# Performance work log

Measured on AMD Instinct MI355X. Metric: run time of the kernel, lower is better.

## Reference

```python
import jax, jax.numpy as jnp
from jax import lax
import numpy as np

_BN_SCALE = 1.0 / float(np.sqrt(1.0 + 1e-5))  # eval BN: running_mean=0, running_var=1
SEMANTIC_GROUPS = [
    ("head_spine", [0, 1, 2, 3, 20]),
    ("left_arm", [4, 5, 6, 7, 21, 22]),
    ("right_arm", [8, 9, 10, 11, 23, 24]),
    ("left_leg", [12, 13, 14, 15]),
    ("right_leg", [16, 17, 18, 19]),
]
_SKELETON_EDGES = [(3, 2), (2, 20), (20, 1), (1, 0), (20, 4), (4, 5), (5, 6), (6, 22), (6, 7), (7, 21),
                   (20, 8), (8, 9), (9, 10), (10, 24), (10, 11), (11, 23), (0, 12), (12, 13), (13, 14),
                   (14, 15), (0, 16), (16, 17), (17, 18), (18, 19)]


def _full_adj():
    adj = np.zeros((25, 25))
    for i, j in [(a - 1, b - 1) for a, b in _SKELETON_EDGES]:
        if 0 <= i < 25 and 0 <= j < 25:
            adj[i, j] = 1.0
            adj[j, i] = 1.0
    adj += np.eye(25)
    deg = adj.sum(1, keepdims=True)
    deg[deg == 0] = 1.0
    return adj / deg


def _sub_adj(joints):
    fa = _full_adj()
    sa = fa[np.ix_(joints, joints)].copy()
    n = len(joints)
    if n > 1:
        sa += np.eye(n)
        deg = sa.sum(1)
        for node in np.nonzero(deg == 1.0)[0]:
            if node != 0:
                sa[0, node] = 1.0
                sa[node, 0] = 1.0
    deg = sa.sum(1, keepdims=True)
    deg[deg == 0] = 1.0
    return jnp.asarray((sa / deg).astype(np.float32))


def _bn(y, g, b):
    # eval-mode BatchNorm2d with running stats (0, 1)
    return y * (g * _BN_SCALE)[None, :, None, None] + b[None, :, None, None]


def _st_layer(x, adj, sw, sb, tw, tb, g, b, res):
    # x: (B, Cin, T, V); sw: (3*Cout, Cin); tw: (Cout, Cout, 3, 1)
    if res is None:
        r = x
    else:
        rw, rb, rg, rbb = res
        r = _bn(jnp.einsum('oc,bctv->botv', rw, x) + rb[None, :, None, None], rg, rbb)
    xg = jnp.einsum('uv,bctv->bctu', adj, x)  # adjacency message passing
    y = jnp.einsum('oc,bctv->botv', sw, xg) + sb[None, :, None, None]
    B, oc3, T, V = y.shape
    y = y.reshape(B, 3, oc3 // 3, T, V).sum(axis=1)  # sum spatial kernel partitions
    y = lax.conv_general_dilated(y, tw, (1, 1), ((1, 1), (0, 0))) + tb[None, :, None, None]
    return jax.nn.relu(_bn(y + r, g, b))


def _vq(inp, cb):
    # inp: (B, D), cb: (K, D); straight-through VQ with commitment_cost=0.25
    d = jnp.sum(inp * inp, 1, keepdims=True) + jnp.sum(cb * cb, 1) - 2.0 * (inp @ cb.T)
    idx = jnp.argmin(d, axis=1)
    q = cb[idx]
    sg = lax.stop_gradient
    loss = jnp.mean((q - sg(inp)) ** 2) + 0.25 * jnp.mean((sg(q) - inp) ** 2)
    return inp + sg(q - inp), loss, idx


def _forward(x, embed_w, embed_b, p1, p2, p3, codebooks):
    h = jnp.einsum('btvc,oc->btvo', x, embed_w) + embed_b  # (B,T,25,64)
    h = h.transpose(0, 3, 1, 2)  # (B,64,T,25)
    quants, losses, idxs = [], [], []
    for gi, (_, joints) in enumerate(SEMANTIC_GROUPS):
        adj = _sub_adj(joints)
        y = h[:, :, :, np.asarray(joints)]
        sw1, sb1, tw1, tb1, g1, b1 = [p[gi] for p in p1]
        y = _st_layer(y, adj, sw1, sb1, tw1, tb1, g1, b1, None)
        rw2, rb2, rg2, rbb2, sw2, sb2, tw2, tb2, g2, b2 = [p[gi] for p in p2]
        y = _st_layer(y, adj, sw2, sb2, tw2, tb2, g2, b2, (rw2, rb2, rg2, rbb2))
        rw3, rb3, rg3, rbb3, sw3, sb3, tw3, tb3, g3, b3 = [p[gi] for p in p3]
        y = _st_layer(y, adj, sw3, sb3, tw3, tb3, g3, b3, (rw3, rb3, rg3, rbb3))
        feat = y.mean(axis=(2, 3))  # AdaptiveAvgPool2d((1,1))
        q, l, i = _vq(feat, codebooks[gi])
        quants.append(q)
        losses.append(l)
        idxs.append(i)
    return jnp.stack(quants), jnp.sum(jnp.stack(losses)), jnp.stack(idxs)


def setup_inputs() -> dict:
    ks = iter(jax.random.split(jax.random.key(0), 48))

    def rn(shape, scale=0.05):
        return jax.random.normal(next(ks), shape, jnp.float32) * scale

    return {
        "x": jax.random.normal(next(ks), (64, 256, 25, 3), jnp.float32),
        "embed_w": rn((64, 3), 0.3),
        "embed_b": rn((64,), 0.01),
        "sgcn_w1": rn((5, 192, 64)),
        "sgcn_b1": rn((5, 192), 0.01),
        "tconv_w1": rn((5, 64, 64, 3, 1)),
        "tconv_b1": rn((5, 64), 0.01),
        "bn_g1": jnp.ones((5, 64), jnp.float32),
        "bn_b1": jnp.zeros((5, 64), jnp.float32),
        "res_w2": rn((5, 128, 64)),
        "res_b2": rn((5, 128), 0.01),
        "resbn_g2": jnp.ones((5, 128), jnp.float32),
        "resbn_b2": jnp.zeros((5, 128), jnp.float32),
        "sgcn_w2": rn((5, 384, 64)),
        "sgcn_b2": rn((5, 384), 0.01),
        "tconv_w2": rn((5, 128, 128, 3, 1)),
        "tconv_b2": rn((5, 128), 0.01),
        "bn_g2": jnp.ones((5, 128), jnp.float32),
        "bn_b2": jnp.zeros((5, 128), jnp.float32),
        "res_w3": rn((5, 64, 128)),
        "res_b3": rn((5, 64), 0.01),
        "resbn_g3": jnp.ones((5, 64), jnp.float32),
        "resbn_b3": jnp.zeros((5, 64), jnp.float32),
        "sgcn_w3": rn((5, 192, 128)),
        "sgcn_b3": rn((5, 192), 0.01),
        "tconv_w3": rn((5, 64, 64, 3, 1)),
        "tconv_b3": rn((5, 64), 0.01),
        "bn_g3": jnp.ones((5, 64), jnp.float32),
        "bn_b3": jnp.zeros((5, 64), jnp.float32),
        "codebooks": jax.random.uniform(next(ks), (5, 128, 64), jnp.float32, -1.0 / 128, 1.0 / 128),
    }


def reference(x, embed_w, embed_b, sgcn_w1, sgcn_b1, tconv_w1, tconv_b1, bn_g1, bn_b1,
              res_w2, res_b2, resbn_g2, resbn_b2, sgcn_w2, sgcn_b2, tconv_w2, tconv_b2, bn_g2, bn_b2,
              res_w3, res_b3, resbn_g3, resbn_b3, sgcn_w3, sgcn_b3, tconv_w3, tconv_b3, bn_g3, bn_b3,
              codebooks):
    p1 = (sgcn_w1, sgcn_b1, tconv_w1, tconv_b1, bn_g1, bn_b1)
    p2 = (res_w2, res_b2, resbn_g2, resbn_b2, sgcn_w2, sgcn_b2, tconv_w2, tconv_b2, bn_g2, bn_b2)
    p3 = (res_w3, res_b3, resbn_g3, resbn_b3, sgcn_w3, sgcn_b3, tconv_w3, tconv_b3, bn_g3, bn_b3)
    return _forward(x, embed_w, embed_b, p1, p2, p3, codebooks)
```

## Files before the change

kernel.cpp:

```cpp
#include <hip/hip_runtime.h>

#define T_ 256
#define B_ 64
static constexpr float BNS = 0.9999950000374997f;

__device__ __constant__ int d_perm[25] = {0,1,2,3,20, 4,5,6,7,21,22, 8,9,10,11,23,24, 12,13,14,15, 16,17,18,19};
__device__ __constant__ int d_gstart[5] = {0,5,11,17,21};
__device__ __constant__ int d_gn[5] = {5,6,6,4,4};
__device__ __constant__ int d_edges[21][2] = {
  {2,1},{1,19},{19,0},{19,3},{3,4},{4,5},{5,21},{5,6},{6,20},{19,7},
  {7,8},{8,9},{9,23},{9,10},{10,22},{11,12},{12,13},{13,14},{15,16},{16,17},{17,18}};

__global__ void adj_kernel(float* __restrict__ adjout){
  if (threadIdx.x != 0 || blockIdx.x != 0) return;
  double fa[25][25];
  for (int i=0;i<25;i++) for (int j=0;j<25;j++) fa[i][j]=0.0;
  for (int e=0;e<21;e++){ int i=d_edges[e][0], j=d_edges[e][1]; fa[i][j]=1.0; fa[j][i]=1.0; }
  for (int i=0;i<25;i++) fa[i][i] += 1.0;
  for (int i=0;i<25;i++){
    double dg=0; for (int j=0;j<25;j++) dg += fa[i][j];
    if (dg==0.0) dg=1.0;
    for (int j=0;j<25;j++) fa[i][j] /= dg;
  }
  for (int g=0; g<5; g++){
    int n = d_gn[g]; int gs = d_gstart[g];
    for (int q=0;q<36;q++) adjout[g*36+q] = 0.f;
    double sa[6][6];
    for (int a=0;a<n;a++) for (int b=0;b<n;b++) sa[a][b] = fa[d_perm[gs+a]][d_perm[gs+b]];
    for (int a=0;a<n;a++) sa[a][a] += 1.0;
    double deg[6];
    for (int a=0;a<n;a++){ double s=0; for (int b=0;b<n;b++) s += sa[a][b]; deg[a]=s; }
    for (int a=1;a<n;a++) if (deg[a]==1.0){ sa[0][a]=1.0; sa[a][0]=1.0; }
    for (int a=0;a<n;a++){
      double s=0; for (int b=0;b<n;b++) s += sa[a][b];
      if (s==0.0) s=1.0;
      for (int b=0;b<n;b++) adjout[g*36 + a*n + b] = (float)(sa[a][b]/s);
    }
  }
}

__global__ void zero_kernel(float* __restrict__ feat, float* __restrict__ loss){
  int i = blockIdx.x*256 + threadIdx.x;
  if (i < 5*64*64) feat[i] = 0.f;
  if (i == 0) loss[0] = 0.f;
}

__global__ __launch_bounds__(256) void fold_swe(
    const float* __restrict__ sw1, const float* __restrict__ sw2, const float* __restrict__ sw3,
    float* __restrict__ swe1, float* __restrict__ swe2, float* __restrict__ swe3){
  int i = blockIdx.x*256 + threadIdx.x;
  if (i < 20480){ int g=i/4096, r=i%4096;
    swe1[i] = sw1[g*12288 + r] + sw1[g*12288 + 4096 + r] + sw1[g*12288 + 8192 + r];
  } else if (i < 61440){ int j=i-20480; int g=j/8192, r=j%8192;
    swe2[j] = sw2[g*24576 + r] + sw2[g*24576 + 8192 + r] + sw2[g*24576 + 16384 + r];
  } else if (i < 102400){ int j=i-61440; int g=j/8192, r=j%8192;
    swe3[j] = sw3[g*24576 + r] + sw3[g*24576 + 8192 + r] + sw3[g*24576 + 16384 + r];
  }
}

template<int Cm, int Cout>
__global__ __launch_bounds__(256) void transpose_tw(const float* __restrict__ tw, float* __restrict__ twT){
  int e = blockIdx.x*256 + threadIdx.x;
  if (e >= 5*3*Cm*Cout) return;
  int o = e % Cout;
  int t = e / Cout;
  int m = t % Cm; t /= Cm;
  int k = t % 3; int g = t/3;
  twT[e] = tw[(size_t)g*Cout*Cm*3 + (o*Cm+m)*3 + k];
}

template<int Cm, int Cin, int Cout>
__global__ __launch_bounds__(256) void prep_gemm(
    const float* __restrict__ twT, const float* __restrict__ swe,
    const float* __restrict__ bg, float* __restrict__ WC){
  constexpr int CT = 256/Cout;
  __shared__ float sS[Cm*CT];
  int g = blockIdx.x, k = blockIdx.y, cz = blockIdx.z;
  int tid = threadIdx.x;
  for (int i=tid; i<Cm*CT; i+=256){
    int m = i/CT, cc = i%CT;
    sS[i] = swe[(size_t)g*Cm*Cin + m*Cin + cz*CT + cc];
  }
  __syncthreads();
  int o = tid % Cout, cc = tid / Cout;
  const float* tp = twT + ((size_t)(g*3+k)*Cm)*Cout + o;
  float acc = 0.f;
  #pragma unroll 4
  for (int m=0;m<Cm;m++) acc += tp[(size_t)m*Cout]*sS[m*CT+cc];
  int c = cz*CT + cc;
  WC[(size_t)g*3*Cin*Cout + ((size_t)k*Cin + c)*Cout + o] = bg[g*Cout+o]*BNS*acc;
}

__global__ __launch_bounds__(256) void prep_rw(
    const float* __restrict__ rw2, const float* __restrict__ rg2, const float* __restrict__ bg2,
    const float* __restrict__ rw3, const float* __restrict__ rg3, const float* __restrict__ bg3,
    float* __restrict__ RW2, float* __restrict__ RW3){
  int i = blockIdx.x*256 + threadIdx.x;
  if (i < 40960){ int g=i/8192, r=i%8192, c=r>>7, o=r&127;
    RW2[i] = bg2[g*128+o]*BNS*rg2[g*128+o]*BNS*rw2[(size_t)g*8192 + o*64 + c];
  } else if (i < 81920){ int j=i-40960; int g=j/8192, r=j%8192, c=r>>6, o=r&63;
    RW3[j] = bg3[g*64+o]*BNS*rg3[g*64+o]*BNS*rw3[(size_t)g*8192 + o*128 + c];
  }
}

__global__ __launch_bounds__(128) void prep_bias(
    const float* __restrict__ twT1, const float* __restrict__ twT2, const float* __restrict__ twT3,
    const float* __restrict__ sb1, const float* __restrict__ tb1, const float* __restrict__ bg1, const float* __restrict__ bb1,
    const float* __restrict__ sb2, const float* __restrict__ tb2, const float* __restrict__ bg2, const float* __restrict__ bb2,
    const float* __restrict__ rb2, const float* __restrict__ rg2, const float* __restrict__ rbb2,
    const float* __restrict__ sb3, const float* __restrict__ tb3, const float* __restrict__ bg3, const float* __restrict__ bb3,
    const float* __restrict__ rb3, const float* __restrict__ rg3, const float* __restrict__ rbb3,
    float* __restrict__ B1, float* __restrict__ RS1, float* __restrict__ B2, float* __restrict__ B3){
  __shared__ float sbe[128];
  int g = blockIdx.x, L = blockIdx.y, tid = threadIdx.x;
  if (L == 0){
    if (tid<64) sbe[tid] = sb1[g*192+tid] + sb1[g*192+64+tid] + sb1[g*192+128+tid];
    __syncthreads();
    if (tid<64){ int o=tid; float gsc = bg1[g*64+o]*BNS;
      for (int k=0;k<3;k++){ float s=0.f; const float* tp = twT1 + ((size_t)(g*3+k)*64)*64 + o;
        for (int m=0;m<64;m++) s += tp[m*64]*sbe[m];
        B1[g*256+(k+1)*64+o] = gsc*s; }
      B1[g*256+o] = gsc*tb1[g*64+o] + bb1[g*64+o];
      RS1[g*64+o] = gsc;
    }
  } else if (L == 1){
    sbe[tid] = sb2[g*384+tid] + sb2[g*384+128+tid] + sb2[g*384+256+tid];
    __syncthreads();
    { int o=tid; float gsc = bg2[g*128+o]*BNS; float rgs = rg2[g*128+o]*BNS;
      for (int k=0;k<3;k++){ float s=0.f; const float* tp = twT2 + ((size_t)(g*3+k)*128)*128 + o;
        for (int m=0;m<128;m++) s += tp[m*128]*sbe[m];
        B2[g*512+(k+1)*128+o] = gsc*s; }
      B2[g*512+o] = gsc*(tb2[g*128+o] + rgs*rb2[g*128+o] + rbb2[g*128+o]) + bb2[g*128+o];
    }
  } else {
    if (tid<64) sbe[tid] = sb3[g*192+tid] + sb3[g*192+64+tid] + sb3[g*192+128+tid];
    __syncthreads();
    if (tid<64){ int o=tid; float gsc = bg3[g*64+o]*BNS; float rgs = rg3[g*64+o]*BNS;
      for (int k=0;k<3;k++){ float s=0.f; const float* tp = twT3 + ((size_t)(g*3+k)*64)*64 + o;
        for (int m=0;m<64;m++) s += tp[m*64]*sbe[m];
        B3[g*256+(k+1)*64+o] = gsc*s; }
      B3[g*256+o] = gsc*(tb3[g*64+o] + rgs*rb3[g*64+o] + rbb3[g*64+o]) + bb3[g*64+o];
    }
  }
}

template<int Cin, int Cout, int NJ, int MODE>
__global__ __launch_bounds__(256) void st_layer(
    const float* __restrict__ in, float* __restrict__ out,
    const float* __restrict__ W, const float* __restrict__ RW,
    const float* __restrict__ BV, const float* __restrict__ RS,
    const float* __restrict__ adjg, const float* __restrict__ ew,
    const float* __restrict__ eb, int gstart)
{
  constexpr int TC = 16;
  constexpr int SE = (TC+2)*NJ;
  constexpr int SITES = TC*NJ;
  constexpr int SP = SITES/8;
  constexpr int OP = Cout/32;
  __shared__ float sIn[SE*Cin];
  __shared__ float sXg[SE*Cin];
  __shared__ float sAdj[NJ*NJ];
  const int tid = threadIdx.x;
  const int b = blockIdx.y;
  const int t0 = blockIdx.x*TC;
  if (tid < NJ*NJ) sAdj[tid] = adjg[tid];

  if (MODE == 1){
    for (int e=tid; e<SE*3; e+=256){
      int se = e/3, j = e - se*3;
      int tl = se/NJ; int u = se - tl*NJ; int t = t0 + tl - 1;
      float v = 0.f;
      if (t>=0 && t<T_){ int joint = d_perm[gstart+u]; v = in[(((size_t)b*T_ + t)*25 + joint)*3 + j]; }
      sXg[e] = v;
    }
    __syncthreads();
    { int c = tid & 63;
      float w0 = ew[c*3], w1 = ew[c*3+1], w2 = ew[c*3+2], b0 = eb[c];
      for (int e=tid; e<SE*64; e+=256){
        int se = e>>6; int t = t0 + se/NJ - 1;
        float v = 0.f;
        if (t>=0 && t<T_) v = b0 + sXg[se*3]*w0 + sXg[se*3+1]*w1 + sXg[se*3+2]*w2;
        sIn[e] = v;
      }
    }
    __syncthreads();
  } else {
    constexpr int NV = SE*Cin/4;
    for (int e4=tid; e4<NV; e4+=256){
      int idx = e4*4;
      int se = idx/Cin; int cc = idx - se*Cin;
      int tl = se/NJ; int u = se - tl*NJ; int t = t0 + tl - 1;
      float4 v = make_float4(0.f,0.f,0.f,0.f);
      if (t>=0 && t<T_) v = *(const float4*)&in[(((size_t)b*T_ + t)*NJ + u)*Cin + cc];
      *(float4*)&sIn[idx] = v;
    }
    __syncthreads();
  }
  for (int e=tid; e<SE*Cin; e+=256){
    int se = e/Cin; int c = e - se*Cin;
    int u = se % NJ; int base = (se-u)*Cin + c;
    float a = 0.f;
    #pragma unroll
    for (int v=0; v<NJ; v++) a += sAdj[u*NJ+v]*sIn[base + v*Cin];
    sXg[e] = a;
  }
  __syncthreads();

  const int lane = tid & 63;
  const int o = lane & 31;
  const int sg = (tid>>6)*2 + (lane>>5);
  const int s0 = sg*SP;

  float acc[SP][OP];
  {
    float bno[OP], bk0[OP], bk1[OP], bk2[OP];
    #pragma unroll
    for (int j=0;j<OP;j++){ int oj = o + j*32;
      bno[j]=BV[oj]; bk0[j]=BV[Cout+oj]; bk1[j]=BV[2*Cout+oj]; bk2[j]=BV[3*Cout+oj]; }
    #pragma unroll
    for (int i=0;i<SP;i++){
      int s = s0 + i; int tg = t0 + s/NJ;
      #pragma unroll
      for (int j=0;j<OP;j++)
        acc[i][j] = bno[j] + bk1[j] + (tg>0 ? bk0[j] : 0.f) + (tg<T_-1 ? bk2[j] : 0.f);
    }
  }
  #pragma unroll 1
  for (int k=0;k<3;k++){
    const float* Wk = W + k*Cin*Cout;
    #pragma unroll 2
    for (int c4=0;c4<Cin;c4+=4){
      float wv[4][OP];
      #pragma unroll
      for (int q=0;q<4;q++)
        #pragma unroll
        for (int j=0;j<OP;j++) wv[q][j] = Wk[(c4+q)*Cout + o + j*32];
      #pragma unroll
      for (int i=0;i<SP;i++){
        const float4 xv = *(const float4*)&sXg[(s0+i+k*NJ)*Cin + c4];
        #pragma unroll
        for (int j=0;j<OP;j++)
          acc[i][j] += xv.x*wv[0][j] + xv.y*wv[1][j] + xv.z*wv[2][j] + xv.w*wv[3][j];
      }
    }
  }
  if (MODE == 1){
    float rsv[OP];
    #pragma unroll
    for (int j=0;j<OP;j++) rsv[j] = RS[o + j*32];
    #pragma unroll
    for (int i=0;i<SP;i++)
      #pragma unroll
      for (int j=0;j<OP;j++)
        acc[i][j] += sIn[(s0+i+NJ)*Cin + o + j*32]*rsv[j];
  } else {
    #pragma unroll 2
    for (int c4=0;c4<Cin;c4+=4){
      float rv[4][OP];
      #pragma unroll
      for (int q=0;q<4;q++)
        #pragma unroll
        for (int j=0;j<OP;j++) rv[q][j] = RW[(c4+q)*Cout + o + j*32];
      #pragma unroll
      for (int i=0;i<SP;i++){
        const float4 xv = *(const float4*)&sIn[(s0+i+NJ)*Cin + c4];
        #pragma unroll
        for (int j=0;j<OP;j++)
          acc[i][j] += xv.x*rv[0][j] + xv.y*rv[1][j] + xv.z*rv[2][j] + xv.w*rv[3][j];
      }
    }
  }
  if (MODE == 3){
    #pragma unroll
    for (int j=0;j<OP;j++){
      float sum = 0.f;
      #pragma unroll
      for (int i=0;i<SP;i++) sum += fmaxf(acc[i][j], 0.f);
      atomicAdd(&out[(size_t)b*64 + o + j*32], sum);
    }
  } else {
    size_t obase = ((size_t)b*T_ + t0)*NJ*Cout;
    #pragma unroll
    for (int i=0;i<SP;i++)
      #pragma unroll
      for (int j=0;j<OP;j++)
        out[obase + (size_t)(s0+i)*Cout + o + j*32] = fmaxf(acc[i][j], 0.f);
  }
}

__global__ __launch_bounds__(128) void vq_kernel(const float* __restrict__ feat,
    const float* __restrict__ cb, float* __restrict__ dout){
  int b = blockIdx.x, g = blockIdx.y, tid = threadIdx.x;
  __shared__ float sF[64];
  __shared__ float sD[128]; __shared__ int sI[128];
  __shared__ float sL[64];
  float inv = 1.0f/(256.0f*(float)d_gn[g]);
  if (tid < 64) sF[tid] = feat[((size_t)g*64 + b)*64 + tid]*inv;
  __syncthreads();
  const float* cbg = cb + (size_t)g*128*64;
  {
    const float* c = cbg + (size_t)tid*64;
    float d = 0.f;
    for (int i=0;i<64;i++){ float df = c[i]-sF[i]; d += df*df; }
    sD[tid] = d; sI[tid] = tid;
  }
  __syncthreads();
  for (int s=64; s>0; s>>=1){
    if (tid < s){
      float d2 = sD[tid+s]; int i2 = sI[tid+s];
      if (d2 < sD[tid] || (d2 == sD[tid] && i2 < sI[tid])){ sD[tid]=d2; sI[tid]=i2; }
    }
    __syncthreads();
  }
  int idx = sI[0];
  if (tid < 64){
    float q = cbg[(size_t)idx*64 + tid];
    dout[((size_t)g*64 + b)*64 + tid] = q;
    float df = q - sF[tid];
    sL[tid] = df*df;
  }
  __syncthreads();
  if (tid == 0){
    float s = 0.f;
    for (int i=0;i<64;i++) s += sL[i];
    atomicAdd(dout + 20480, 1.25f*s/4096.0f);
    dout[20481 + g*64 + b] = (float)idx;
  }
}

static void launch_st1(int nj, dim3 grid, hipStream_t s, const float* x, float* A1,
    const float* WC, const float* BV, const float* RS, const float* adj,
    const float* ew, const float* eb, int gstart){
  switch(nj){
    case 4: st_layer<64,64,4,1><<<grid,256,0,s>>>(x,A1,WC,nullptr,BV,RS,adj,ew,eb,gstart); break;
    case 5: st_layer<64,64,5,1><<<grid,256,0,s>>>(x,A1,WC,nullptr,BV,RS,adj,ew,eb,gstart); break;
    case 6: st_layer<64,64,6,1><<<grid,256,0,s>>>(x,A1,WC,nullptr,BV,RS,adj,ew,eb,gstart); break;
  }
}
static void launch_st2(int nj, dim3 grid, hipStream_t s, const float* A1, float* A2,
    const float* WC, const float* RW, const float* BV, const float* adj){
  switch(nj){
    case 4: st_layer<64,128,4,2><<<grid,256,0,s>>>(A1,A2,WC,RW,BV,nullptr,adj,nullptr,nullptr,0); break;
    case 5: st_layer<64,128,5,2><<<grid,256,0,s>>>(A1,A2,WC,RW,BV,nullptr,adj,nullptr,nullptr,0); break;
    case 6: st_layer<64,128,6,2><<<grid,256,0,s>>>(A1,A2,WC,RW,BV,nullptr,adj,nullptr,nullptr,0); break;
  }
}
static void launch_st3(int nj, dim3 grid, hipStream_t s, const float* A2, float* featg,
    const float* WC, const float* RW, const float* BV, const float* adj){
  switch(nj){
    case 4: st_layer<128,64,4,3><<<grid,256,0,s>>>(A2,featg,WC,RW,BV,nullptr,adj,nullptr,nullptr,0); break;
    case 5: st_layer<128,64,5,3><<<grid,256,0,s>>>(A2,featg,WC,RW,BV,nullptr,adj,nullptr,nullptr,0); break;
    case 6: st_layer<128,64,6,3><<<grid,256,0,s>>>(A2,featg,WC,RW,BV,nullptr,adj,nullptr,nullptr,0); break;
  }
}

extern "C" void kernel_launch(void* const* d_in, const int* in_sizes, int n_in,
                              void* d_out, int out_size, void* d_ws, size_t ws_size,
                              hipStream_t stream) {
  const float* x    = (const float*)d_in[0];
  const float* ew   = (const float*)d_in[1];
  const float* eb   = (const float*)d_in[2];
  const float* sw1  = (const float*)d_in[3];
  const float* sb1  = (const float*)d_in[4];
  const float* tw1  = (const float*)d_in[5];
  const float* tb1  = (const float*)d_in[6];
  const float* bg1  = (const float*)d_in[7];
  const float* bb1  = (const float*)d_in[8];
  const float* rw2  = (const float*)d_in[9];
  const float* rb2  = (const float*)d_in[10];
  const float* rg2  = (const float*)d_in[11];
  const float* rbb2 = (const float*)d_in[12];
  const float* sw2  = (const float*)d_in[13];
  const float* sb2  = (const float*)d_in[14];
  const float* tw2  = (const float*)d_in[15];
  const float* tb2  = (const float*)d_in[16];
  const float* bg2  = (const float*)d_in[17];
  const float* bb2  = (const float*)d_in[18];
  const float* rw3  = (const float*)d_in[19];
  const float* rb3  = (const float*)d_in[20];
  const float* rg3  = (const float*)d_in[21];
  const float* rbb3 = (const float*)d_in[22];
  const float* sw3  = (const float*)d_in[23];
  const float* sb3  = (const float*)d_in[24];
  const float* tw3  = (const float*)d_in[25];
  const float* tb3  = (const float*)d_in[26];
  const float* bg3  = (const float*)d_in[27];
  const float* bb3  = (const float*)d_in[28];
  const float* cbs  = (const float*)d_in[29];
  float* dout = (float*)d_out;
  float* ws = (float*)d_ws;

  const size_t OFF_ADJ = 0;
  const size_t OFF_WC1 = 256;
  const size_t OFF_B1  = 61696;
  const size_t OFF_RS1 = 62976;
  const size_t OFF_WC2 = 63296;
  const size_t OFF_RW2 = 186176;
  const size_t OFF_B2  = 227136;
  const size_t OFF_WC3 = 229696;
  const size_t OFF_RW3 = 352576;
  const size_t OFF_B3  = 393536;
  const size_t OFF_FEAT= 394816;
  const size_t OFF_A1  = 415296;
  const size_t OFF_A2  = 6706752;
  const size_t WS_FLOATS = 19289664;
  if (ws_size < WS_FLOATS*sizeof(float)) return;

  float* adj5 = ws + OFF_ADJ;
  float* WC1  = ws + OFF_WC1;  float* B1 = ws + OFF_B1;  float* RS1 = ws + OFF_RS1;
  float* WC2  = ws + OFF_WC2;  float* RW2 = ws + OFF_RW2; float* B2 = ws + OFF_B2;
  float* WC3  = ws + OFF_WC3;  float* RW3 = ws + OFF_RW3; float* B3 = ws + OFF_B3;
  float* feat = ws + OFF_FEAT;
  float* A1   = ws + OFF_A1;
  float* A2   = ws + OFF_A2;

  float* twT1 = A2;
  float* twT2 = A2 + 61440;
  float* twT3 = A2 + 307200;
  float* swe1 = A2 + 368640;
  float* swe2 = A2 + 389120;
  float* swe3 = A2 + 430080;

  zero_kernel<<<80, 256, 0, stream>>>(feat, dout + 20480);
  adj_kernel<<<1, 64, 0, stream>>>(adj5);
  fold_swe<<<400, 256, 0, stream>>>(sw1, sw2, sw3, swe1, swe2, swe3);
  transpose_tw<64,64>  <<<240, 256, 0, stream>>>(tw1, twT1);
  transpose_tw<128,128><<<960, 256, 0, stream>>>(tw2, twT2);
  transpose_tw<64,64>  <<<240, 256, 0, stream>>>(tw3, twT3);
  prep_gemm<64,64,64>  <<<dim3(5,3,16), 256, 0, stream>>>(twT1, swe1, bg1, WC1);
  prep_gemm<128,64,128><<<dim3(5,3,32), 256, 0, stream>>>(twT2, swe2, bg2, WC2);
  prep_gemm<64,128,64> <<<dim3(5,3,32), 256, 0, stream>>>(twT3, swe3, bg3, WC3);
  prep_rw<<<320, 256, 0, stream>>>(rw2, rg2, bg2, rw3, rg3, bg3, RW2, RW3);
  prep_bias<<<dim3(5,3), 128, 0, stream>>>(twT1, twT2, twT3,
      sb1, tb1, bg1, bb1,
      sb2, tb2, bg2, bb2, rb2, rg2, rbb2,
      sb3, tb3, bg3, bb3, rb3, rg3, rbb3,
      B1, RS1, B2, B3);

  const int h_gn[5] = {5,6,6,4,4};
  const int h_gstart[5] = {0,5,11,17,21};
  dim3 grid(T_/16, B_);
  for (int g=0; g<5; g++){
    int nj = h_gn[g];
    launch_st1(nj, grid, stream, x, A1, WC1 + (size_t)g*12288, B1 + g*256, RS1 + g*64,
               adj5 + g*36, ew, eb, h_gstart[g]);
    launch_st2(nj, grid, stream, A1, A2, WC2 + (size_t)g*24576, RW2 + (size_t)g*8192,
               B2 + g*512, adj5 + g*36);
    launch_st3(nj, grid, stream, A2, feat + (size_t)g*4096, WC3 + (size_t)g*24576,
               RW3 + (size_t)g*8192, B3 + g*256, adj5 + g*36);
  }
  vq_kernel<<<dim3(B_,5), 128, 0, stream>>>(feat, cbs, dout);
}
```

Before: 1.699 ms.

## Chunk input channels by 32 and split layer-2 outputs across grid z

```diff
diff --git a/kernel.cpp b/kernel.cpp
--- a/kernel.cpp
+++ b/kernel.cpp
@@ -144,8 +144,8 @@
   }
 }
 
-template<int Cin, int Cout, int NJ, int MODE>
-__global__ __launch_bounds__(256) void st_layer(
+template<int Cin, int COS, int NJ, int MODE>
+__global__ __launch_bounds__(256, 4) void st_layer(
     const float* __restrict__ in, float* __restrict__ out,
     const float* __restrict__ W, const float* __restrict__ RW,
     const float* __restrict__ BV, const float* __restrict__ RS,
@@ -156,55 +156,30 @@
   constexpr int SE = (TC+2)*NJ;
   constexpr int SITES = TC*NJ;
   constexpr int SP = SITES/8;
-  constexpr int OP = Cout/32;
-  __shared__ float sIn[SE*Cin];
-  __shared__ float sXg[SE*Cin];
+  constexpr int OP = 2;
+  constexpr int NCH = Cin/32;
+  __shared__ float sIn[SE*32];
+  __shared__ float sXg[SE*32];
   __shared__ float sAdj[NJ*NJ];
+  __shared__ float sX3[MODE==1 ? SE*3 : 1];
   const int tid = threadIdx.x;
   const int b = blockIdx.y;
   const int t0 = blockIdx.x*TC;
+  const int ooff = blockIdx.z*64;
+  W += ooff; BV += ooff;
+  if (MODE != 1) RW += ooff;
+  if (MODE == 2) out += ooff;
+
   if (tid < NJ*NJ) sAdj[tid] = adjg[tid];
-
   if (MODE == 1){
     for (int e=tid; e<SE*3; e+=256){
       int se = e/3, j = e - se*3;
       int tl = se/NJ; int u = se - tl*NJ; int t = t0 + tl - 1;
       float v = 0.f;
       if (t>=0 && t<T_){ int joint = d_perm[gstart+u]; v = in[(((size_t)b*T_ + t)*25 + joint)*3 + j]; }
-      sXg[e] = v;
-    }
-    __syncthreads();
-    { int c = tid & 63;
-      float w0 = ew[c*3], w1 = ew[c*3+1], w2 = ew[c*3+2], b0 = eb[c];
-      for (int e=tid; e<SE*64; e+=256){
-        int se = e>>6; int t = t0 + se/NJ - 1;
-        float v = 0.f;
-        if (t>=0 && t<T_) v = b0 + sXg[se*3]*w0 + sXg[se*3+1]*w1 + sXg[se*3+2]*w2;
-        sIn[e] = v;
-      }
-    }
-    __syncthreads();
-  } else {
-    constexpr int NV = SE*Cin/4;
-    for (int e4=tid; e4<NV; e4+=256){
-      int idx = e4*4;
-      int se = idx/Cin; int cc = idx - se*Cin;
-      int tl = se/NJ; int u = se - tl*NJ; int t = t0 + tl - 1;
-      float4 v = make_float4(0.f,0.f,0.f,0.f);
-      if (t>=0 && t<T_) v = *(const float4*)&in[(((size_t)b*T_ + t)*NJ + u)*Cin + cc];
-      *(float4*)&sIn[idx] = v;
-    }
-    __syncthreads();
-  }
-  for (int e=tid; e<SE*Cin; e+=256){
-    int se = e/Cin; int c = e - se*Cin;
-    int u = se % NJ; int base = (se-u)*Cin + c;
-    float a = 0.f;
-    #pragma unroll
-    for (int v=0; v<NJ; v++) a += sAdj[u*NJ+v]*sIn[base + v*Cin];
-    sXg[e] = a;
-  }
-  __syncthreads();
+      sX3[e] = v;
+    }
+  }
 
   const int lane = tid & 63;
   const int o = lane & 31;
@@ -215,8 +190,8 @@
   {
     float bno[OP], bk0[OP], bk1[OP], bk2[OP];
     #pragma unroll
-    for (int j=0;j<OP;j++){ int oj = o + j*32;
-      bno[j]=BV[oj]; bk0[j]=BV[Cout+oj]; bk1[j]=BV[2*Cout+oj]; bk2[j]=BV[3*Cout+oj]; }
+    for (int j=0;j<OP;j++){ int oj = j*32 + o;
+      bno[j]=BV[oj]; bk0[j]=BV[COS+oj]; bk1[j]=BV[2*COS+oj]; bk2[j]=BV[3*COS+oj]; }
     #pragma unroll
     for (int i=0;i<SP;i++){
       int s = s0 + i; int tg = t0 + s/NJ;
@@ -225,48 +200,76 @@
         acc[i][j] = bno[j] + bk1[j] + (tg>0 ? bk0[j] : 0.f) + (tg<T_-1 ? bk2[j] : 0.f);
     }
   }
+
   #pragma unroll 1
-  for (int k=0;k<3;k++){
-    const float* Wk = W + k*Cin*Cout;
-    #pragma unroll 2
-    for (int c4=0;c4<Cin;c4+=4){
-      float wv[4][OP];
+  for (int cz=0; cz<NCH; ++cz){
+    __syncthreads();
+    if (MODE == 1){
+      int cg = cz*32 + (tid & 31);
+      float w0 = ew[cg*3], w1 = ew[cg*3+1], w2 = ew[cg*3+2], b0 = eb[cg];
+      for (int e=tid; e<SE*32; e+=256){
+        int se = e>>5; int t = t0 + se/NJ - 1;
+        float v = 0.f;
+        if (t>=0 && t<T_) v = b0 + sX3[se*3]*w0 + sX3[se*3+1]*w1 + sX3[se*3+2]*w2;
+        sIn[e] = v;
+      }
+    } else {
+      for (int e4=tid; e4<SE*8; e4+=256){
+        int se = e4>>3; int cc = (e4&7)<<2;
+        int tl = se/NJ; int u = se - tl*NJ; int t = t0 + tl - 1;
+        float4 v = make_float4(0.f,0.f,0.f,0.f);
+        if (t>=0 && t<T_) v = *(const float4*)&in[(((size_t)b*T_ + t)*NJ + u)*(size_t)Cin + cz*32 + cc];
+        *(float4*)&sIn[se*32+cc] = v;
+      }
+    }
+    __syncthreads();
+    for (int e=tid; e<SE*32; e+=256){
+      int se = e>>5; int c = e&31; int u = se%NJ; int base = (se-u)*32 + c;
+      float a = 0.f;
       #pragma unroll
-      for (int q=0;q<4;q++)
+      for (int v=0; v<NJ; v++) a += sAdj[u*NJ+v]*sIn[base + v*32];
+      sXg[e] = a;
+    }
+    __syncthreads();
+    #pragma unroll 1
+    for (int k=0;k<3;k++){
+      const float* Wk = W + (size_t)(k*Cin + cz*32)*COS;
+      #pragma unroll 2
+      for (int c4=0;c4<32;c4+=4){
+        float wv[4][OP];
         #pragma unroll
-        for (int j=0;j<OP;j++) wv[q][j] = Wk[(c4+q)*Cout + o + j*32];
+        for (int q=0;q<4;q++)
+          #pragma unroll
+          for (int j=0;j<OP;j++) wv[q][j] = Wk[(size_t)(c4+q)*COS + j*32 + o];
+        #pragma unroll
+        for (int i=0;i<SP;i++){
+          const float4 xv = *(const float4*)&sXg[(s0+i+k*NJ)*32 + c4];
+          #pragma unroll
+          for (int j=0;j<OP;j++)
+            acc[i][j] += xv.x*wv[0][j] + xv.y*wv[1][j] + xv.z*wv[2][j] + xv.w*wv[3][j];
+        }
+      }
+    }
+    if (MODE == 1){
+      float rsv = RS[cz*32 + o];
       #pragma unroll
-      for (int i=0;i<SP;i++){
-        const float4 xv = *(const float4*)&sXg[(s0+i+k*NJ)*Cin + c4];
+      for (int i=0;i<SP;i++)
+        acc[i][cz] += sIn[(s0+i+NJ)*32 + o]*rsv;
+    } else {
+      #pragma unroll 2
+      for (int c4=0;c4<32;c4+=4){
+        float rv[4][OP];
         #pragma unroll
-        for (int j=0;j<OP;j++)
-          acc[i][j] += xv.x*wv[0][j] + xv.y*wv[1][j] + xv.z*wv[2][j] + xv.w*wv[3][j];
-      }
-    }
-  }
-  if (MODE == 1){
-    float rsv[OP];
-    #pragma unroll
-    for (int j=0;j<OP;j++) rsv[j] = RS[o + j*32];
-    #pragma unroll
-    for (int i=0;i<SP;i++)
-      #pragma unroll
-      for (int j=0;j<OP;j++)
-        acc[i][j] += sIn[(s0+i+NJ)*Cin + o + j*32]*rsv[j];
-  } else {
-    #pragma unroll 2
-    for (int c4=0;c4<Cin;c4+=4){
-      float rv[4][OP];
-      #pragma unroll
-      for (int q=0;q<4;q++)
+        for (int q=0;q<4;q++)
+          #pragma unroll
+          for (int j=0;j<OP;j++) rv[q][j] = RW[(size_t)(cz*32+c4+q)*COS + j*32 + o];
         #pragma unroll
-        for (int j=0;j<OP;j++) rv[q][j] = RW[(c4+q)*Cout + o + j*32];
-      #pragma unroll
-      for (int i=0;i<SP;i++){
-        const float4 xv = *(const float4*)&sIn[(s0+i+NJ)*Cin + c4];
-        #pragma unroll
-        for (int j=0;j<OP;j++)
-          acc[i][j] += xv.x*rv[0][j] + xv.y*rv[1][j] + xv.z*rv[2][j] + xv.w*rv[3][j];
+        for (int i=0;i<SP;i++){
+          const float4 xv = *(const float4*)&sIn[(s0+i+NJ)*32 + c4];
+          #pragma unroll
+          for (int j=0;j<OP;j++)
+            acc[i][j] += xv.x*rv[0][j] + xv.y*rv[1][j] + xv.z*rv[2][j] + xv.w*rv[3][j];
+        }
       }
     }
   }
@@ -276,15 +279,15 @@
       float sum = 0.f;
       #pragma unroll
       for (int i=0;i<SP;i++) sum += fmaxf(acc[i][j], 0.f);
-      atomicAdd(&out[(size_t)b*64 + o + j*32], sum);
+      atomicAdd(&out[(size_t)b*64 + j*32 + o], sum);
     }
   } else {
-    size_t obase = ((size_t)b*T_ + t0)*NJ*Cout;
+    size_t obase = ((size_t)b*T_ + t0)*NJ*COS;
     #pragma unroll
     for (int i=0;i<SP;i++)
       #pragma unroll
       for (int j=0;j<OP;j++)
-        out[obase + (size_t)(s0+i)*Cout + o + j*32] = fmaxf(acc[i][j], 0.f);
+        out[obase + (size_t)(s0+i)*COS + j*32 + o] = fmaxf(acc[i][j], 0.f);
   }
 }
 
@@ -328,25 +331,28 @@
   }
 }
 
-static void launch_st1(int nj, dim3 grid, hipStream_t s, const float* x, float* A1,
+static void launch_st1(int nj, hipStream_t s, const float* x, float* A1,
     const float* WC, const float* BV, const float* RS, const float* adj,
     const float* ew, const float* eb, int gstart){
+  dim3 grid(T_/16, B_, 1);
   switch(nj){
     case 4: st_layer<64,64,4,1><<<grid,256,0,s>>>(x,A1,WC,nullptr,BV,RS,adj,ew,eb,gstart); break;
     case 5: st_layer<64,64,5,1><<<grid,256,0,s>>>(x,A1,WC,nullptr,BV,RS,adj,ew,eb,gstart); break;
     case 6: st_layer<64,64,6,1><<<grid,256,0,s>>>(x,A1,WC,nullptr,BV,RS,adj,ew,eb,gstart); break;
   }
 }
-static void launch_st2(int nj, dim3 grid, hipStream_t s, const float* A1, float* A2,
+static void launch_st2(int nj, hipStream_t s, const float* A1, float* A2,
     const float* WC, const float* RW, const float* BV, const float* adj){
+  dim3 grid(T_/16, B_, 2);
   switch(nj){
     case 4: st_layer<64,128,4,2><<<grid,256,0,s>>>(A1,A2,WC,RW,BV,nullptr,adj,nullptr,nullptr,0); break;
     case 5: st_layer<64,128,5,2><<<grid,256,0,s>>>(A1,A2,WC,RW,BV,nullptr,adj,nullptr,nullptr,0); break;
     case 6: st_layer<64,128,6,2><<<grid,256,0,s>>>(A1,A2,WC,RW,BV,nullptr,adj,nullptr,nullptr,0); break;
   }
 }
-static void launch_st3(int nj, dim3 grid, hipStream_t s, const float* A2, float* featg,
+static void launch_st3(int nj, hipStream_t s, const float* A2, float* featg,
     const float* WC, const float* RW, const float* BV, const float* adj){
+  dim3 grid(T_/16, B_, 1);
   switch(nj){
     case 4: st_layer<128,64,4,3><<<grid,256,0,s>>>(A2,featg,WC,RW,BV,nullptr,adj,nullptr,nullptr,0); break;
     case 5: st_layer<128,64,5,3><<<grid,256,0,s>>>(A2,featg,WC,RW,BV,nullptr,adj,nullptr,nullptr,0); break;
@@ -439,14 +445,13 @@
 
   const int h_gn[5] = {5,6,6,4,4};
   const int h_gstart[5] = {0,5,11,17,21};
-  dim3 grid(T_/16, B_);
   for (int g=0; g<5; g++){
     int nj = h_gn[g];
-    launch_st1(nj, grid, stream, x, A1, WC1 + (size_t)g*12288, B1 + g*256, RS1 + g*64,
+    launch_st1(nj, stream, x, A1, WC1 + (size_t)g*12288, B1 + g*256, RS1 + g*64,
                adj5 + g*36, ew, eb, h_gstart[g]);
-    launch_st2(nj, grid, stream, A1, A2, WC2 + (size_t)g*24576, RW2 + (size_t)g*8192,
+    launch_st2(nj, stream, A1, A2, WC2 + (size_t)g*24576, RW2 + (size_t)g*8192,
                B2 + g*512, adj5 + g*36);
-    launch_st3(nj, grid, stream, A2, feat + (size_t)g*4096, WC3 + (size_t)g*24576,
+    launch_st3(nj, stream, A2, feat + (size_t)g*4096, WC3 + (size_t)g*24576,
                RW3 + (size_t)g*8192, B3 + g*256, adj5 + g*36);
   }
   vq_kernel<<<dim3(B_,5), 128, 0, stream>>>(feat, cbs, dout);
```

Result: no change. 1.712 ms (+0.8%).
